# Optimization experiments

Hardware: AMD Instinct MI355X
Metric: run time of the kernel (lower is better)

Reference implementation:

```python
import jax, jax.numpy as jnp
import numpy as np

EMBED_DIM = 1024
NUM_HEADS = 16
DEPTH = EMBED_DIM // NUM_HEADS  # 64
B, S = 4, 2048


def setup_inputs() -> dict:
    key = jax.random.key(0)
    ks = jax.random.split(key, 12)
    sc = 0.02
    return {
        "q": jax.random.normal(ks[0], (B, S, EMBED_DIM), jnp.float32),
        "k": jax.random.normal(ks[1], (B, S, EMBED_DIM), jnp.float32),
        "v": jax.random.normal(ks[2], (B, S, EMBED_DIM), jnp.float32),
        # per-head Dense(depth) weights stacked over heads: [H, D, depth]
        "wq": jax.random.normal(ks[3], (NUM_HEADS, EMBED_DIM, DEPTH), jnp.float32) * sc,
        "bq": jnp.zeros((NUM_HEADS, DEPTH), jnp.float32),
        "wk": jax.random.normal(ks[4], (NUM_HEADS, EMBED_DIM, DEPTH), jnp.float32) * sc,
        "bk": jnp.zeros((NUM_HEADS, DEPTH), jnp.float32),
        "wv": jax.random.normal(ks[5], (NUM_HEADS, EMBED_DIM, DEPTH), jnp.float32) * sc,
        "bv": jnp.zeros((NUM_HEADS, DEPTH), jnp.float32),
        # final Dense(embedding_dim): [D, D]
        "wo": jax.random.normal(ks[6], (EMBED_DIM, EMBED_DIM), jnp.float32) * sc,
        "bo": jnp.zeros((EMBED_DIM,), jnp.float32),
        "use_mask": 1,
    }


def reference(q, k, v, wq, bq, wk, bk, wv, bv, wo, bo, use_mask):
    # Batched per-head projections (equivalent to H separate Dense layers).
    qh = jnp.einsum('bsd,hde->bhse', q, wq) + bq[None, :, None, :]
    kh = jnp.einsum('bsd,hde->bhse', k, wk) + bk[None, :, None, :]
    vh = jnp.einsum('bsd,hde->bhse', v, wv) + bv[None, :, None, :]

    scale = 1.0 / jnp.sqrt(jnp.asarray(DEPTH, jnp.float32))
    logits = jnp.einsum('bhqe,bhke->bhqk', qh, kh) * scale  # [B,H,Sq,Sk]
    if use_mask:
        Sq, Sk = qh.shape[2], kh.shape[2]
        causal = jnp.triu(jnp.ones((Sq, Sk), jnp.float32), k=1)
        logits = logits + causal[None, None, :, :] * (-1e9)
    attn = jax.nn.softmax(logits, axis=-1)
    out_h = jnp.einsum('bhqk,bhke->bhqe', attn, vh)  # [B,H,Sq,depth]
    # concat heads along last dim -> [B,Sq,H*depth]
    bsz, H, Sq, dep = out_h.shape
    concat = out_h.transpose(0, 2, 1, 3).reshape(bsz, Sq, H * dep)
    return concat @ wo + bo
```

## Files before the change

kernel.cpp:

```cpp
#include <hip/hip_runtime.h>

#define B_ 4
#define S_ 2048
#define H_ 16
#define D_ 64
#define E_ 1024
#define M_ 8192

typedef __attribute__((ext_vector_type(8))) __bf16 bf16x8;
typedef __attribute__((ext_vector_type(4))) __bf16 bf16x4;
typedef __attribute__((ext_vector_type(4))) float f32x4;
typedef __attribute__((ext_vector_type(16))) float f32x16;

__device__ __forceinline__ void gload_lds16(const void* g, void* l) {
  __builtin_amdgcn_global_load_lds(
      (const __attribute__((address_space(1))) unsigned int*)g,
      (__attribute__((address_space(3))) unsigned int*)l, 16, 0, 0);
}

__device__ __forceinline__ unsigned pk2(float a, float b) {
  union { __bf16 h; unsigned short u; } ua, ub;
  ua.h = (__bf16)a; ub.h = (__bf16)b;
  return ((unsigned)ub.u << 16) | (unsigned)ua.u;
}

__global__ void cvt_all(const float* __restrict__ q, const float* __restrict__ k,
                        const float* __restrict__ v, __bf16* __restrict__ Aq,
                        __bf16* __restrict__ Ak, __bf16* __restrict__ Av) {
  const int y = blockIdx.y;
  const float* src = (y == 0) ? q : (y == 1) ? k : v;
  __bf16* dst = (y == 0) ? Aq : (y == 1) ? Ak : Av;
  const int i = blockIdx.x * blockDim.x + threadIdx.x;
  const float4 vv = ((const float4*)src)[i];
  bf16x4 o;
  o.x = (__bf16)vv.x; o.y = (__bf16)vv.y; o.z = (__bf16)vv.z; o.w = (__bf16)vv.w;
  ((bf16x4*)dst)[i] = o;
}

__global__ void pack_all(const float* __restrict__ wq, const float* __restrict__ wk,
                         const float* __restrict__ wv, const float* __restrict__ wo,
                         __bf16* __restrict__ Bq, __bf16* __restrict__ Bk,
                         __bf16* __restrict__ Bv, __bf16* __restrict__ Bo) {
  const int y = blockIdx.y;
  const int idx = blockIdx.x * 256 + threadIdx.x;
  const int n = idx >> 10, kk = idx & 1023;
  if (y < 3) {
    const float* w = (y == 0) ? wq : (y == 1) ? wk : wv;
    __bf16* out = (y == 0) ? Bq : (y == 1) ? Bk : Bv;
    out[idx] = (__bf16)w[((size_t)(n >> 6) << 16) + (kk << 6) + (n & 63)];
  } else {
    Bo[idx] = (__bf16)wo[((size_t)kk << 10) + n];
  }
}

__global__ __launch_bounds__(256) void gemm_qk(
    const __bf16* __restrict__ Aq, const __bf16* __restrict__ Ak,
    const __bf16* __restrict__ Bq, const __bf16* __restrict__ Bk,
    const float* __restrict__ bq, const float* __restrict__ bk,
    __bf16* __restrict__ qhb, __bf16* __restrict__ khb) {
  constexpr int K = 1024;
  __shared__ __bf16 As[128 * 64];
  __shared__ __bf16 Bs[128 * 64];
  const int t = threadIdx.x;
  const int w = t >> 6, l = t & 63;
  const int isK = blockIdx.y >> 3;
  const __bf16* A = isK ? Ak : Aq;
  const __bf16* Bt = isK ? Bk : Bq;
  const float* bias = isK ? bk : bq;
  __bf16* C = isK ? khb : qhb;
  const int m0 = blockIdx.x * 128, n0 = (blockIdx.y & 7) * 128;
  f32x4 acc[4][4] = {};

  for (int kt = 0; kt < K / 64; ++kt) {
    const int kb = kt * 64;
#pragma unroll
    for (int j = 0; j < 4; ++j) {
      const int ci = (j * 4 + w) * 64 + l;
      const int row = ci >> 3;
      const int c = (ci & 7) ^ (row & 7);
      gload_lds16(A + (size_t)(m0 + row) * K + kb + c * 8, As + (j * 4 + w) * 512);
      gload_lds16(Bt + (size_t)(n0 + row) * K + kb + c * 8, Bs + (j * 4 + w) * 512);
    }
    __syncthreads();
#pragma unroll
    for (int kk = 0; kk < 64; kk += 32) {
      bf16x8 af[4], bfr[4];
#pragma unroll
      for (int f = 0; f < 4; ++f) {
        const int ra = (w >> 1) * 64 + f * 16 + (l & 15);
        const int ca = ((kk >> 3) + (l >> 4)) ^ (ra & 7);
        af[f] = *(const bf16x8*)(As + ra * 64 + ca * 8);
        const int rb = (w & 1) * 64 + f * 16 + (l & 15);
        const int cb = ((kk >> 3) + (l >> 4)) ^ (rb & 7);
        bfr[f] = *(const bf16x8*)(Bs + rb * 64 + cb * 8);
      }
#pragma unroll
      for (int mf = 0; mf < 4; ++mf)
#pragma unroll
        for (int nf = 0; nf < 4; ++nf)
          acc[mf][nf] = __builtin_amdgcn_mfma_f32_16x16x32_bf16(af[mf], bfr[nf],
                                                                acc[mf][nf], 0, 0, 0);
    }
    __syncthreads();
  }

#pragma unroll
  for (int mf = 0; mf < 4; ++mf)
#pragma unroll
    for (int nf = 0; nf < 4; ++nf)
#pragma unroll
      for (int r = 0; r < 4; ++r) {
        const int gm = m0 + (w >> 1) * 64 + mf * 16 + (l >> 4) * 4 + r;
        const int gn = n0 + (w & 1) * 64 + nf * 16 + (l & 15);
        const float val = acc[mf][nf][r] + bias[gn];
        C[(((size_t)(gm >> 11) * H_ + (gn >> 6)) * S_ + (gm & 2047)) * D_ + (gn & 63)] =
            (__bf16)val;
      }
}

template <int MODE>
__global__ __launch_bounds__(256) void gemm_bt(const __bf16* __restrict__ A,
                                               const __bf16* __restrict__ Bt,
                                               const float* __restrict__ bias,
                                               void* __restrict__ Cout) {
  constexpr int K = 1024;
  __shared__ __bf16 As[128 * 64];
  __shared__ __bf16 Bs[128 * 64];
  const int t = threadIdx.x;
  const int w = t >> 6, l = t & 63;
  const int m0 = blockIdx.x * 128, n0 = blockIdx.y * 128;
  f32x4 acc[4][4] = {};

  for (int kt = 0; kt < K / 64; ++kt) {
    const int kb = kt * 64;
#pragma unroll
    for (int j = 0; j < 4; ++j) {
      const int ci = (j * 4 + w) * 64 + l;
      const int row = ci >> 3;
      const int c = (ci & 7) ^ (row & 7);
      gload_lds16(A + (size_t)(m0 + row) * K + kb + c * 8, As + (j * 4 + w) * 512);
      gload_lds16(Bt + (size_t)(n0 + row) * K + kb + c * 8, Bs + (j * 4 + w) * 512);
    }
    __syncthreads();
#pragma unroll
    for (int kk = 0; kk < 64; kk += 32) {
      bf16x8 af[4], bfr[4];
#pragma unroll
      for (int f = 0; f < 4; ++f) {
        const int ra = (w >> 1) * 64 + f * 16 + (l & 15);
        const int ca = ((kk >> 3) + (l >> 4)) ^ (ra & 7);
        af[f] = *(const bf16x8*)(As + ra * 64 + ca * 8);
        const int rb = (w & 1) * 64 + f * 16 + (l & 15);
        const int cb = ((kk >> 3) + (l >> 4)) ^ (rb & 7);
        bfr[f] = *(const bf16x8*)(Bs + rb * 64 + cb * 8);
      }
#pragma unroll
      for (int mf = 0; mf < 4; ++mf)
#pragma unroll
        for (int nf = 0; nf < 4; ++nf)
          acc[mf][nf] = __builtin_amdgcn_mfma_f32_16x16x32_bf16(af[mf], bfr[nf],
                                                                acc[mf][nf], 0, 0, 0);
    }
    __syncthreads();
  }

#pragma unroll
  for (int mf = 0; mf < 4; ++mf) {
#pragma unroll
    for (int nf = 0; nf < 4; ++nf) {
#pragma unroll
      for (int r = 0; r < 4; ++r) {
        const int gm = m0 + (w >> 1) * 64 + mf * 16 + (l >> 4) * 4 + r;
        const int gn = n0 + (w & 1) * 64 + nf * 16 + (l & 15);
        const float val = acc[mf][nf][r] + ((MODE == 1) ? bias[gm] : bias[gn]);
        if constexpr (MODE == 1) {
          ((__bf16*)Cout)[(((size_t)(gn >> 11) * H_ + (gm >> 6)) * D_ + (gm & 63)) * S_ + (gn & 2047)] =
              (__bf16)val;
        } else {
          ((float*)Cout)[(size_t)gm * 1024 + gn] = val;
        }
      }
    }
  }
}

__device__ __forceinline__ void stage_k128(const __bf16* __restrict__ Kb, int kt,
                                           __bf16* Kdst, int t, int w) {
#pragma unroll
  for (int j = 0; j < 4; ++j) {
    const int ci = j * 256 + t;
    const int row = ci >> 3;
    const int sc = (ci & 7) ^ (row & 7);
    gload_lds16(Kb + (size_t)(kt * 128 + row) * D_ + sc * 8, Kdst + j * 2048 + w * 512);
  }
}
__device__ __forceinline__ void stage_v64(const __bf16* __restrict__ Vb, int col0,
                                          __bf16* Vdst, int t, int w) {
#pragma unroll
  for (int j = 0; j < 2; ++j) {
    const int ci = j * 256 + t;
    const int row = ci >> 3;
    const int sc = (ci & 7) ^ (row & 7);
    gload_lds16(Vb + (size_t)row * S_ + col0 + sc * 8, Vdst + j * 2048 + w * 512);
  }
}

__global__ __launch_bounds__(256, 2) void attn_fused(const __bf16* __restrict__ qh,
                                                     const __bf16* __restrict__ kh,
                                                     const __bf16* __restrict__ vT,
                                                     __bf16* __restrict__ concat,
                                                     const int* __restrict__ use_mask_p) {
  __shared__ __bf16 Ks[2][128 * 64];
  __shared__ __bf16 Vs[2][2][64 * 64];
  const int t = threadIdx.x, w = t >> 6, l = t & 63;
  const int lo = l & 31, hi = l >> 5;
  const int bh = blockIdx.x, pr = blockIdx.y;
  const int usemask = *use_mask_p;
  const __bf16* Qb = qh + (size_t)bh * S_ * D_;
  const __bf16* Kb = kh + (size_t)bh * S_ * D_;
  const __bf16* Vb = vT + (size_t)bh * D_ * S_;
  const int b = bh >> 4, hh = bh & 15;
  constexpr float CEXP = 0.125f * 1.4426950408889634f;

  bf16x8 ones;
#pragma unroll
  for (int i = 0; i < 8; ++i) ones[i] = (__bf16)1.0f;

  int cur = 0;
  for (int half = 0; half < 2; ++half) {
    const int qt = half ? (15 - pr) : pr;
    const int qrow0 = qt * 128 + w * 32;
    const int nkt = usemask ? (qt + 1) : (S_ / 128);
    const int ktw = usemask ? (2 * qt + (w >> 1)) : (1 << 30);

    bf16x8 qf[4];
#pragma unroll
    for (int ks = 0; ks < 4; ++ks)
      qf[ks] = *(const bf16x8*)(Qb + (size_t)(qrow0 + lo) * D_ + ks * 16 + hi * 8);

    float m = -3e38f;
    f32x16 lsacc = {};
    f32x16 o0 = {}, o1 = {};

    stage_k128(Kb, 0, &Ks[cur][0], t, w);
    stage_v64(Vb, 0, &Vs[cur][0][0], t, w);
    stage_v64(Vb, 64, &Vs[cur][1][0], t, w);

    for (int kt = 0; kt < nkt; ++kt) {
      __builtin_amdgcn_sched_barrier(0);
      asm volatile("s_waitcnt vmcnt(0)" ::: "memory");
      __builtin_amdgcn_s_barrier();
      __builtin_amdgcn_sched_barrier(0);

      if (kt + 1 < nkt) {
        const int nxt = cur ^ 1;
        stage_k128(Kb, kt + 1, &Ks[nxt][0], t, w);
        stage_v64(Vb, (kt + 1) * 128, &Vs[nxt][0][0], t, w);
        stage_v64(Vb, (kt + 1) * 128 + 64, &Vs[nxt][1][0], t, w);
      }

#pragma unroll
      for (int sub = 0; sub < 2; ++sub) {
        const int st = 2 * kt + sub;
        if (st <= ktw) {
          const __bf16* Ksub = &Ks[cur][sub * 64 * 64];
          const __bf16* Vsub = &Vs[cur][sub][0];

          f32x16 s0 = {}, s1 = {};
          __builtin_amdgcn_s_setprio(1);
#pragma unroll
          for (int ks = 0; ks < 4; ++ks) {
            const int ch = ((ks << 1) | hi) ^ (lo & 7);
            const bf16x8 k0 = *(const bf16x8*)(Ksub + lo * 64 + ch * 8);
            const bf16x8 k1 = *(const bf16x8*)(Ksub + (32 + lo) * 64 + ch * 8);
            s0 = __builtin_amdgcn_mfma_f32_32x32x16_bf16(k0, qf[ks], s0, 0, 0, 0);
            s1 = __builtin_amdgcn_mfma_f32_32x32x16_bf16(k1, qf[ks], s1, 0, 0, 0);
          }
          __builtin_amdgcn_s_setprio(0);

          if (usemask && st == ktw) {
            const int qloc = ((w & 1) << 5) + lo;
#pragma unroll
            for (int r = 0; r < 16; ++r) {
              const int kv0 = (r & 3) + 8 * (r >> 2) + 4 * hi;
              if (kv0 > qloc) s0[r] = -1e30f;
              if (kv0 + 32 > qloc) s1[r] = -1e30f;
            }
          }

          float pm = s0[0];
#pragma unroll
          for (int r = 1; r < 16; ++r) pm = fmaxf(pm, s0[r]);
#pragma unroll
          for (int r = 0; r < 16; ++r) pm = fmaxf(pm, s1[r]);

          if (!__all(pm - m <= 64.0f)) {
            const float pmp = fmaxf(pm, __shfl_xor(pm, 32));
            const float mn = fmaxf(m, pmp);
            const float al = __builtin_amdgcn_exp2f((m - mn) * CEXP);
            m = mn;
            lsacc[0] *= al;
            o0 *= al;
            o1 *= al;
          }
          const float mneg = -m * CEXP;

          unsigned W0[4][2], W1[4][2];
#pragma unroll
          for (int j = 0; j < 4; ++j) {
            float p0 = __builtin_amdgcn_exp2f(__builtin_fmaf(s0[4 * j + 0], CEXP, mneg));
            float p1 = __builtin_amdgcn_exp2f(__builtin_fmaf(s0[4 * j + 1], CEXP, mneg));
            float p2 = __builtin_amdgcn_exp2f(__builtin_fmaf(s0[4 * j + 2], CEXP, mneg));
            float p3 = __builtin_amdgcn_exp2f(__builtin_fmaf(s0[4 * j + 3], CEXP, mneg));
            W0[j][0] = pk2(p0, p1);
            W0[j][1] = pk2(p2, p3);
            float q0 = __builtin_amdgcn_exp2f(__builtin_fmaf(s1[4 * j + 0], CEXP, mneg));
            float q1 = __builtin_amdgcn_exp2f(__builtin_fmaf(s1[4 * j + 1], CEXP, mneg));
            float q2 = __builtin_amdgcn_exp2f(__builtin_fmaf(s1[4 * j + 2], CEXP, mneg));
            float q3 = __builtin_amdgcn_exp2f(__builtin_fmaf(s1[4 * j + 3], CEXP, mneg));
            W1[j][0] = pk2(q0, q1);
            W1[j][1] = pk2(q2, q3);
          }

          bf16x8 pa[4];
#pragma unroll
          for (int ks = 0; ks < 4; ++ks) {
            const int c = ks & 1;
            unsigned x0, x1, y0, y1;
            if ((ks >> 1) == 0) {
              x0 = W0[2 * c][0]; x1 = W0[2 * c][1];
              y0 = W0[2 * c + 1][0]; y1 = W0[2 * c + 1][1];
            } else {
              x0 = W1[2 * c][0]; x1 = W1[2 * c][1];
              y0 = W1[2 * c + 1][0]; y1 = W1[2 * c + 1][1];
            }
            asm volatile("v_permlane32_swap_b32 %0, %1" : "+v"(x0), "+v"(y0));
            asm volatile("v_permlane32_swap_b32 %0, %1" : "+v"(x1), "+v"(y1));
            union { unsigned u[4]; bf16x8 v; } uu;
            uu.u[0] = x0; uu.u[1] = x1; uu.u[2] = y0; uu.u[3] = y1;
            pa[ks] = uu.v;
          }

          __builtin_amdgcn_s_setprio(1);
#pragma unroll
          for (int ks = 0; ks < 4; ++ks) {
            const int ch = ((ks << 1) | hi) ^ (lo & 7);
            const bf16x8 v0 = *(const bf16x8*)(Vsub + lo * 64 + ch * 8);
            const bf16x8 v1 = *(const bf16x8*)(Vsub + (32 + lo) * 64 + ch * 8);
            o0 = __builtin_amdgcn_mfma_f32_32x32x16_bf16(v0, pa[ks], o0, 0, 0, 0);
            o1 = __builtin_amdgcn_mfma_f32_32x32x16_bf16(v1, pa[ks], o1, 0, 0, 0);
            lsacc = __builtin_amdgcn_mfma_f32_32x32x16_bf16(ones, pa[ks], lsacc, 0, 0, 0);
          }
          __builtin_amdgcn_s_setprio(0);
        }
      }
      cur ^= 1;
    }

    const float inv = 1.0f / lsacc[0];
    const size_t rowbase = ((size_t)(b * S_ + qrow0 + lo)) * E_ + hh * 64;
#pragma unroll
    for (int rr = 0; rr < 4; ++rr) {
      bf16x4 v0, v1;
#pragma unroll
      for (int bb = 0; bb < 4; ++bb) {
        v0[bb] = (__bf16)(o0[4 * rr + bb] * inv);
        v1[bb] = (__bf16)(o1[4 * rr + bb] * inv);
      }
      *(bf16x4*)(concat + rowbase + 8 * rr + 4 * hi) = v0;
      *(bf16x4*)(concat + rowbase + 32 + 8 * rr + 4 * hi) = v1;
    }
  }
}

extern "C" void kernel_launch(void* const* d_in, const int* in_sizes, int n_in,
                              void* d_out, int out_size, void* d_ws, size_t ws_size,
                              hipStream_t stream) {
  const float* q = (const float*)d_in[0];
  const float* k = (const float*)d_in[1];
  const float* v = (const float*)d_in[2];
  const float* wq = (const float*)d_in[3];
  const float* bq = (const float*)d_in[4];
  const float* wk = (const float*)d_in[5];
  const float* bk = (const float*)d_in[6];
  const float* wv = (const float*)d_in[7];
  const float* bv = (const float*)d_in[8];
  const float* wo = (const float*)d_in[9];
  const float* bo = (const float*)d_in[10];
  const int* use_mask = (const int*)d_in[11];
  (void)in_sizes; (void)n_in; (void)out_size; (void)ws_size;

  char* ws = (char*)d_ws;
  __bf16* Aq = (__bf16*)ws;
  __bf16* Ak = Aq + (size_t)M_ * E_;
  __bf16* Av = Ak + (size_t)M_ * E_;
  __bf16* Bq = Av + (size_t)M_ * E_;
  __bf16* Bk = Bq + (size_t)E_ * E_;
  __bf16* Bv = Bk + (size_t)E_ * E_;
  __bf16* Bo = Bv + (size_t)E_ * E_;
  __bf16* qhb = Bo + (size_t)E_ * E_;
  __bf16* khb = qhb + (size_t)8388608;
  __bf16* vTb = khb + (size_t)8388608;
  __bf16* concat = Aq;

  cvt_all<<<dim3(8192, 3), 256, 0, stream>>>(q, k, v, Aq, Ak, Av);
  pack_all<<<dim3(4096, 4), 256, 0, stream>>>(wq, wk, wv, wo, Bq, Bk, Bv, Bo);
  gemm_qk<<<dim3(64, 16), 256, 0, stream>>>(Aq, Ak, Bq, Bk, bq, bk, qhb, khb);
  gemm_bt<1><<<dim3(8, 64), 256, 0, stream>>>(Bv, Av, bv, vTb);
  attn_fused<<<dim3(64, 8), 256, 0, stream>>>(qhb, khb, vTb, concat, use_mask);
  gemm_bt<2><<<dim3(64, 8), 256, 0, stream>>>(concat, Bo, bo, d_out);
}
```

Baseline: 196.0 us.

## Double-buffer LDS tiles in projection GEMMs to overlap loads with MFMA

Adds a two-stage LDS pipeline to the QK and generic GEMM kernels. The next K-tile is issued via global_load_lds into the alternate buffer before computing on the current one, with a single waitcnt plus barrier per iteration. This targets the global-load latency that was exposed when load and compute ran serially. In exchange it doubles LDS usage to 64KB per block, which may reduce occupancy.

```diff
diff --git a/kernel.cpp b/kernel.cpp
--- a/kernel.cpp
+++ b/kernel.cpp
@@ -53,14 +53,57 @@
   }
 }
 
+#define GEMM_STAGE(A_, Bt_, kt_, buf_)                                        \
+  {                                                                           \
+    const int kb_ = (kt_) * 64;                                               \
+    _Pragma("unroll") for (int j = 0; j < 4; ++j) {                           \
+      const int ci = (j * 4 + w) * 64 + l;                                    \
+      const int row = ci >> 3;                                                \
+      const int c = (ci & 7) ^ (row & 7);                                     \
+      gload_lds16((A_) + (size_t)(m0 + row) * 1024 + kb_ + c * 8,             \
+                  As[buf_] + (j * 4 + w) * 512);                              \
+      gload_lds16((Bt_) + (size_t)(n0 + row) * 1024 + kb_ + c * 8,            \
+                  Bs[buf_] + (j * 4 + w) * 512);                              \
+    }                                                                         \
+  }
+
+#define GEMM_COMPUTE(buf_)                                                    \
+  _Pragma("unroll") for (int kk = 0; kk < 64; kk += 32) {                     \
+    bf16x8 af[4], bfr[4];                                                     \
+    _Pragma("unroll") for (int f = 0; f < 4; ++f) {                           \
+      const int ra = (w >> 1) * 64 + f * 16 + (l & 15);                       \
+      const int ca = ((kk >> 3) + (l >> 4)) ^ (ra & 7);                       \
+      af[f] = *(const bf16x8*)(As[buf_] + ra * 64 + ca * 8);                  \
+      const int rb = (w & 1) * 64 + f * 16 + (l & 15);                        \
+      const int cb = ((kk >> 3) + (l >> 4)) ^ (rb & 7);                       \
+      bfr[f] = *(const bf16x8*)(Bs[buf_] + rb * 64 + cb * 8);                 \
+    }                                                                         \
+    _Pragma("unroll") for (int mf = 0; mf < 4; ++mf)                          \
+        _Pragma("unroll") for (int nf = 0; nf < 4; ++nf)                      \
+            acc[mf][nf] = __builtin_amdgcn_mfma_f32_16x16x32_bf16(            \
+                af[mf], bfr[nf], acc[mf][nf], 0, 0, 0);                       \
+  }
+
+#define GEMM_PIPE(A_, Bt_)                                                    \
+  GEMM_STAGE(A_, Bt_, 0, 0);                                                  \
+  int cur = 0;                                                                \
+  for (int kt = 0; kt < 16; ++kt) {                                           \
+    __builtin_amdgcn_sched_barrier(0);                                        \
+    asm volatile("s_waitcnt vmcnt(0)" ::: "memory");                          \
+    __builtin_amdgcn_s_barrier();                                             \
+    __builtin_amdgcn_sched_barrier(0);                                        \
+    if (kt + 1 < 16) GEMM_STAGE(A_, Bt_, kt + 1, cur ^ 1);                    \
+    GEMM_COMPUTE(cur);                                                        \
+    cur ^= 1;                                                                 \
+  }
+
 __global__ __launch_bounds__(256) void gemm_qk(
     const __bf16* __restrict__ Aq, const __bf16* __restrict__ Ak,
     const __bf16* __restrict__ Bq, const __bf16* __restrict__ Bk,
     const float* __restrict__ bq, const float* __restrict__ bk,
     __bf16* __restrict__ qhb, __bf16* __restrict__ khb) {
-  constexpr int K = 1024;
-  __shared__ __bf16 As[128 * 64];
-  __shared__ __bf16 Bs[128 * 64];
+  __shared__ __bf16 As[2][128 * 64];
+  __shared__ __bf16 Bs[2][128 * 64];
   const int t = threadIdx.x;
   const int w = t >> 6, l = t & 63;
   const int isK = blockIdx.y >> 3;
@@ -71,38 +114,7 @@
   const int m0 = blockIdx.x * 128, n0 = (blockIdx.y & 7) * 128;
   f32x4 acc[4][4] = {};
 
-  for (int kt = 0; kt < K / 64; ++kt) {
-    const int kb = kt * 64;
-#pragma unroll
-    for (int j = 0; j < 4; ++j) {
-      const int ci = (j * 4 + w) * 64 + l;
-      const int row = ci >> 3;
-      const int c = (ci & 7) ^ (row & 7);
-      gload_lds16(A + (size_t)(m0 + row) * K + kb + c * 8, As + (j * 4 + w) * 512);
-      gload_lds16(Bt + (size_t)(n0 + row) * K + kb + c * 8, Bs + (j * 4 + w) * 512);
-    }
-    __syncthreads();
-#pragma unroll
-    for (int kk = 0; kk < 64; kk += 32) {
-      bf16x8 af[4], bfr[4];
-#pragma unroll
-      for (int f = 0; f < 4; ++f) {
-        const int ra = (w >> 1) * 64 + f * 16 + (l & 15);
-        const int ca = ((kk >> 3) + (l >> 4)) ^ (ra & 7);
-        af[f] = *(const bf16x8*)(As + ra * 64 + ca * 8);
-        const int rb = (w & 1) * 64 + f * 16 + (l & 15);
-        const int cb = ((kk >> 3) + (l >> 4)) ^ (rb & 7);
-        bfr[f] = *(const bf16x8*)(Bs + rb * 64 + cb * 8);
-      }
-#pragma unroll
-      for (int mf = 0; mf < 4; ++mf)
-#pragma unroll
-        for (int nf = 0; nf < 4; ++nf)
-          acc[mf][nf] = __builtin_amdgcn_mfma_f32_16x16x32_bf16(af[mf], bfr[nf],
-                                                                acc[mf][nf], 0, 0, 0);
-    }
-    __syncthreads();
-  }
+  GEMM_PIPE(A, Bt);
 
 #pragma unroll
   for (int mf = 0; mf < 4; ++mf)
@@ -123,46 +135,14 @@
                                                const __bf16* __restrict__ Bt,
                                                const float* __restrict__ bias,
                                                void* __restrict__ Cout) {
-  constexpr int K = 1024;
-  __shared__ __bf16 As[128 * 64];
-  __shared__ __bf16 Bs[128 * 64];
+  __shared__ __bf16 As[2][128 * 64];
+  __shared__ __bf16 Bs[2][128 * 64];
   const int t = threadIdx.x;
   const int w = t >> 6, l = t & 63;
   const int m0 = blockIdx.x * 128, n0 = blockIdx.y * 128;
   f32x4 acc[4][4] = {};
 
-  for (int kt = 0; kt < K / 64; ++kt) {
-    const int kb = kt * 64;
-#pragma unroll
-    for (int j = 0; j < 4; ++j) {
-      const int ci = (j * 4 + w) * 64 + l;
-      const int row = ci >> 3;
-      const int c = (ci & 7) ^ (row & 7);
-      gload_lds16(A + (size_t)(m0 + row) * K + kb + c * 8, As + (j * 4 + w) * 512);
-      gload_lds16(Bt + (size_t)(n0 + row) * K + kb + c * 8, Bs + (j * 4 + w) * 512);
-    }
-    __syncthreads();
-#pragma unroll
-    for (int kk = 0; kk < 64; kk += 32) {
-      bf16x8 af[4], bfr[4];
-#pragma unroll
-      for (int f = 0; f < 4; ++f) {
-        const int ra = (w >> 1) * 64 + f * 16 + (l & 15);
-        const int ca = ((kk >> 3) + (l >> 4)) ^ (ra & 7);
-        af[f] = *(const bf16x8*)(As + ra * 64 + ca * 8);
-        const int rb = (w & 1) * 64 + f * 16 + (l & 15);
-        const int cb = ((kk >> 3) + (l >> 4)) ^ (rb & 7);
-        bfr[f] = *(const bf16x8*)(Bs + rb * 64 + cb * 8);
-      }
-#pragma unroll
-      for (int mf = 0; mf < 4; ++mf)
-#pragma unroll
-        for (int nf = 0; nf < 4; ++nf)
-          acc[mf][nf] = __builtin_amdgcn_mfma_f32_16x16x32_bf16(af[mf], bfr[nf],
-                                                                acc[mf][nf], 0, 0, 0);
-    }
-    __syncthreads();
-  }
+  GEMM_PIPE(A, Bt);
 
 #pragma unroll
   for (int mf = 0; mf < 4; ++mf) {
```

After: 206.5 us. +5.3%, slower.
